# Kernel tuning notes

Measured on AMD Instinct MI355X. Metric: run time of the kernel, lower is better.

## Reference

```python
import jax, jax.numpy as jnp
import numpy as np

D_X = 1024
D_TEXT = 768
FUSION_DIM = D_X + D_TEXT  # 1792
M = 16
K = 2


def setup_inputs() -> dict:
    key = jax.random.key(0)
    k1, k2, k3, k4, k5 = jax.random.split(key, 5)
    B, H, W = 256, 32, 32
    x = jax.random.normal(k1, (B, D_X, H, W), dtype=jnp.float32)
    degraded = jax.random.normal(k2, (B, D_TEXT), dtype=jnp.float32)
    # learned params (random so routing is non-trivial)
    w_fusion = jax.random.normal(k3, (FUSION_DIM, FUSION_DIM), dtype=jnp.float32) * (1.0 / np.sqrt(FUSION_DIM))
    b_fusion = jax.random.normal(k4, (FUSION_DIM,), dtype=jnp.float32) * 0.01
    w_gate = jax.random.normal(k5, (FUSION_DIM, M), dtype=jnp.float32) * 0.02
    return {"x": x, "degraded": degraded, "w_fusion": w_fusion,
            "b_fusion": b_fusion, "w_gate": w_gate}


def reference(x, degraded, w_fusion, b_fusion, w_gate):
    B = x.shape[0]
    # global average pool over H,W -> [B, d_x]
    x_pooled = jnp.mean(x, axis=(2, 3))
    fused = jnp.concatenate([x_pooled, degraded], axis=1)        # [B, d_x+d_text]
    fused = jnp.dot(fused, w_fusion) + b_fusion                  # Linear
    fused = jax.nn.gelu(fused, approximate=False)                # exact GELU (torch default)
    clean_logits = jnp.dot(fused, w_gate)                        # [B, M]
    probs_for_mi = jax.nn.softmax(clean_logits, axis=1)
    # eval path: logits = clean_logits (no noise)
    num_consider = min(K + 1, M)
    top_logits, top_indices = jax.lax.top_k(clean_logits, num_consider)
    top_k_logits = top_logits[:, :K]
    top_k_indices = top_indices[:, :K]
    top_k_gates = jax.nn.softmax(top_k_logits, axis=1)
    rows = jnp.arange(B)[:, None]
    gates = jnp.zeros_like(clean_logits).at[rows, top_k_indices].set(top_k_gates)
    moe_loss = jnp.float32(0.0)
    return gates, moe_loss, probs_for_mi, top_k_indices
```

## Files before the change

kernel.cpp:

```cpp
#include <hip/hip_runtime.h>
#include <math.h>

#define D_X      1024
#define D_TEXT   768
#define FDIM     1792
#define BATCH    256
#define M_EXP    16
#define HW_TOT   1024

#define OUT_GATES 0
#define OUT_LOSS  4096
#define OUT_PROBS 4097
#define OUT_IDX   8193

#define NBLK_DGEMM 224
#define NBLK_POOL  (BATCH * D_X / 4)

__global__ __launch_bounds__(256) void pool_deggemm_kernel(const float* __restrict__ x,
                                                           const float* __restrict__ deg,
                                                           const float* __restrict__ W,
                                                           float* __restrict__ fused,
                                                           float* __restrict__ pact2) {
    __shared__ float As1[32][33];
    __shared__ float Ws1[32][64];

    const int bid = blockIdx.x;
    const int tid = threadIdx.x;

    if (bid >= NBLK_DGEMM) {
        const int gtid = (bid - NBLK_DGEMM) * 256 + tid;
        const int row  = gtid >> 6;
        const int lane = gtid & 63;
        const float4* xr = reinterpret_cast<const float4*>(x + (size_t)row * HW_TOT);
        float s = 0.0f;
#pragma unroll
        for (int k = 0; k < 4; ++k) {
            float4 v = xr[k * 64 + lane];
            s += v.x + v.y + v.z + v.w;
        }
#pragma unroll
        for (int off = 32; off > 0; off >>= 1) s += __shfl_xor(s, off, 64);
        if (lane == 0) fused[row] = s * (1.0f / 1024.0f);
        return;
    }

    const int mb = bid / 28;
    const int nb = bid % 28;
    const int m0 = mb * 32;
    const int n0 = nb * 64;

    const int tx = tid & 15;
    const int ty = tid >> 4;

    const int ar  = tid >> 3;
    const int ak4 = (tid & 7) * 4;
    const int wk  = tid >> 4;
    const int wc4 = (tid & 15) * 4;

    float acc[2][4] = {};

    for (int k0 = 0; k0 < D_TEXT; k0 += 32) {
        __syncthreads();
        {
            const float4 a = *reinterpret_cast<const float4*>(
                deg + (size_t)(m0 + ar) * D_TEXT + k0 + ak4);
            As1[ak4 + 0][ar] = a.x; As1[ak4 + 1][ar] = a.y;
            As1[ak4 + 2][ar] = a.z; As1[ak4 + 3][ar] = a.w;
            *reinterpret_cast<float4*>(&Ws1[wk][wc4]) =
                *reinterpret_cast<const float4*>(W + (size_t)(D_X + k0 + wk) * FDIM + n0 + wc4);
            *reinterpret_cast<float4*>(&Ws1[wk + 16][wc4]) =
                *reinterpret_cast<const float4*>(W + (size_t)(D_X + k0 + wk + 16) * FDIM + n0 + wc4);
        }
        __syncthreads();
#pragma unroll
        for (int kk = 0; kk < 32; ++kk) {
            const float2 a = *reinterpret_cast<const float2*>(&As1[kk][ty * 2]);
            const float4 w = *reinterpret_cast<const float4*>(&Ws1[kk][tx * 4]);
            acc[0][0] = fmaf(a.x, w.x, acc[0][0]);
            acc[0][1] = fmaf(a.x, w.y, acc[0][1]);
            acc[0][2] = fmaf(a.x, w.z, acc[0][2]);
            acc[0][3] = fmaf(a.x, w.w, acc[0][3]);
            acc[1][0] = fmaf(a.y, w.x, acc[1][0]);
            acc[1][1] = fmaf(a.y, w.y, acc[1][1]);
            acc[1][2] = fmaf(a.y, w.z, acc[1][2]);
            acc[1][3] = fmaf(a.y, w.w, acc[1][3]);
        }
    }

#pragma unroll
    for (int i = 0; i < 2; ++i) {
        float4 v;
        v.x = acc[i][0]; v.y = acc[i][1]; v.z = acc[i][2]; v.w = acc[i][3];
        *reinterpret_cast<float4*>(pact2 + (size_t)(m0 + ty * 2 + i) * FDIM + n0 + tx * 4) = v;
    }
}

#define BM 32
#define BN 64
#define BK 64
#define KDIM D_X
#define NITER (KDIM / BK)

#define LOADA(k0)                                                                     \
    pa0 = *reinterpret_cast<const float4*>(A + (size_t)(m0 + ar) * KDIM + (k0) + ak4);       \
    pa1 = *reinterpret_cast<const float4*>(A + (size_t)(m0 + ar + 16) * KDIM + (k0) + ak4);

#define LOADW(k0)                                                                     \
    pw0 = *reinterpret_cast<const float4*>(W + (size_t)((k0) + wr0) * FDIM + n0 + wc4);      \
    pw1 = *reinterpret_cast<const float4*>(W + (size_t)((k0) + wr0 + 16) * FDIM + n0 + wc4); \
    pw2 = *reinterpret_cast<const float4*>(W + (size_t)((k0) + wr0 + 32) * FDIM + n0 + wc4); \
    pw3 = *reinterpret_cast<const float4*>(W + (size_t)((k0) + wr0 + 48) * FDIM + n0 + wc4);

#define STOREA(buf)                                                                   \
    As[buf][ak4 + 0][ar] = pa0.x; As[buf][ak4 + 1][ar] = pa0.y;                       \
    As[buf][ak4 + 2][ar] = pa0.z; As[buf][ak4 + 3][ar] = pa0.w;                       \
    As[buf][ak4 + 0][ar + 16] = pa1.x; As[buf][ak4 + 1][ar + 16] = pa1.y;             \
    As[buf][ak4 + 2][ar + 16] = pa1.z; As[buf][ak4 + 3][ar + 16] = pa1.w;

#define STOREW(buf)                                                                   \
    *reinterpret_cast<float4*>(&Ws[buf][wr0][wc4])      = pw0;                        \
    *reinterpret_cast<float4*>(&Ws[buf][wr0 + 16][wc4]) = pw1;                        \
    *reinterpret_cast<float4*>(&Ws[buf][wr0 + 32][wc4]) = pw2;                        \
    *reinterpret_cast<float4*>(&Ws[buf][wr0 + 48][wc4]) = pw3;

__global__ __launch_bounds__(256) void gemm_gate_kernel(const float* __restrict__ A,
                                                        const float* __restrict__ W,
                                                        const float* __restrict__ pact2,
                                                        const float* __restrict__ bias,
                                                        const float* __restrict__ wg,
                                                        float* __restrict__ part) {
    __shared__ float As[2][BK][BM + 1];
    __shared__ float Ws[2][BK][BN];
    __shared__ float wgs[BN][M_EXP];
    __shared__ float actS[BM][BN + 1];

    const int tid = threadIdx.x;
    const int tx = tid & 15;
    const int ty = tid >> 4;
    const int m0 = blockIdx.x * BM;
    const int n0 = blockIdx.y * BN;

    {
        const int r  = tid >> 2;
        const int c4 = (tid & 3) * 4;
        *reinterpret_cast<float4*>(&wgs[r][c4]) =
            *reinterpret_cast<const float4*>(wg + (size_t)(n0 + r) * M_EXP + c4);
    }

    const int ar  = tid >> 4;
    const int ak4 = (tid & 15) * 4;
    const int wr0 = tid >> 4;
    const int wc4 = (tid & 15) * 4;

    float4 pa0, pa1, pw0, pw1, pw2, pw3;

    LOADA(0); LOADW(0);
    STOREA(0); STOREW(0);
    LOADA(BK); LOADW(BK);

    float acc[2][4];
    {
        const float4 i0 = *reinterpret_cast<const float4*>(
            pact2 + (size_t)(m0 + ty * 2) * FDIM + n0 + tx * 4);
        const float4 i1 = *reinterpret_cast<const float4*>(
            pact2 + (size_t)(m0 + ty * 2 + 1) * FDIM + n0 + tx * 4);
        acc[0][0] = i0.x; acc[0][1] = i0.y; acc[0][2] = i0.z; acc[0][3] = i0.w;
        acc[1][0] = i1.x; acc[1][1] = i1.y; acc[1][2] = i1.z; acc[1][3] = i1.w;
    }
    __syncthreads();

    int cur = 0;
    for (int t = 0; t < NITER; ++t) {
#pragma unroll
        for (int kk = 0; kk < BK; ++kk) {
            const float2 a = *reinterpret_cast<const float2*>(&As[cur][kk][ty * 2]);
            const float4 w = *reinterpret_cast<const float4*>(&Ws[cur][kk][tx * 4]);
            acc[0][0] = fmaf(a.x, w.x, acc[0][0]);
            acc[0][1] = fmaf(a.x, w.y, acc[0][1]);
            acc[0][2] = fmaf(a.x, w.z, acc[0][2]);
            acc[0][3] = fmaf(a.x, w.w, acc[0][3]);
            acc[1][0] = fmaf(a.y, w.x, acc[1][0]);
            acc[1][1] = fmaf(a.y, w.y, acc[1][1]);
            acc[1][2] = fmaf(a.y, w.z, acc[1][2]);
            acc[1][3] = fmaf(a.y, w.w, acc[1][3]);
        }
        if (t < NITER - 1) {
            const int nxt = cur ^ 1;
            STOREA(nxt); STOREW(nxt);
            if (t < NITER - 2) {
                const int k0 = (t + 2) * BK;
                LOADA(k0); LOADW(k0);
            }
            __syncthreads();
            cur = nxt;
        }
    }

#pragma unroll
    for (int i = 0; i < 2; ++i) {
        const int m = ty * 2 + i;
#pragma unroll
        for (int j = 0; j < 4; ++j) {
            const int n = tx * 4 + j;
            const float v = acc[i][j] + bias[n0 + n];
            actS[m][n] = v * 0.5f * (1.0f + erff(v * 0.70710678118654752440f));
        }
    }
    __syncthreads();

    const int pm = tid >> 3;
    const int pe = (tid & 7) * 2;
    float s0 = 0.0f, s1 = 0.0f;
#pragma unroll
    for (int n = 0; n < BN; ++n) {
        const float a = actS[pm][n];
        s0 = fmaf(a, wgs[n][pe], s0);
        s1 = fmaf(a, wgs[n][pe + 1], s1);
    }
    float* pr = part + ((size_t)blockIdx.y * BATCH + m0 + pm) * M_EXP + pe;
    pr[0] = s0;
    pr[1] = s1;
}

#define NNB (FDIM / BN)

__global__ __launch_bounds__(64) void finalize_kernel(const float* __restrict__ part,
                                                      float* __restrict__ out) {
    const int b = blockIdx.x * 64 + threadIdx.x;

    float l[M_EXP];
#pragma unroll
    for (int m = 0; m < M_EXP; ++m) l[m] = 0.0f;

    for (int nb = 0; nb < NNB; ++nb) {
        const float4* pr = reinterpret_cast<const float4*>(part + ((size_t)nb * BATCH + b) * M_EXP);
#pragma unroll
        for (int q = 0; q < 4; ++q) {
            const float4 v = pr[q];
            l[q * 4 + 0] += v.x;
            l[q * 4 + 1] += v.y;
            l[q * 4 + 2] += v.z;
            l[q * 4 + 3] += v.w;
        }
    }

    float mx = l[0];
#pragma unroll
    for (int m = 1; m < M_EXP; ++m) mx = fmaxf(mx, l[m]);
    float e[M_EXP], s = 0.0f;
#pragma unroll
    for (int m = 0; m < M_EXP; ++m) { e[m] = expf(l[m] - mx); s += e[m]; }
    const float inv = 1.0f / s;
#pragma unroll
    for (int m = 0; m < M_EXP; ++m) out[OUT_PROBS + b * M_EXP + m] = e[m] * inv;

    int i0 = 0; float v0 = l[0];
#pragma unroll
    for (int m = 1; m < M_EXP; ++m) if (l[m] > v0) { v0 = l[m]; i0 = m; }
    int i1 = -1; float v1 = -INFINITY;
#pragma unroll
    for (int m = 0; m < M_EXP; ++m) if (m != i0 && l[m] > v1) { v1 = l[m]; i1 = m; }

    const float t = expf(v1 - v0);
    const float g0 = 1.0f / (1.0f + t);
    const float g1 = t * g0;

#pragma unroll
    for (int m = 0; m < M_EXP; ++m) out[OUT_GATES + b * M_EXP + m] = 0.0f;
    out[OUT_GATES + b * M_EXP + i0] = g0;
    out[OUT_GATES + b * M_EXP + i1] = g1;

    out[OUT_IDX + b * 2 + 0] = (float)i0;
    out[OUT_IDX + b * 2 + 1] = (float)i1;

    if (b == 0) out[OUT_LOSS] = 0.0f;
}

extern "C" void kernel_launch(void* const* d_in, const int* in_sizes, int n_in,
                              void* d_out, int out_size, void* d_ws, size_t ws_size,
                              hipStream_t stream) {
    const float* x        = (const float*)d_in[0];
    const float* degraded = (const float*)d_in[1];
    const float* w_fusion = (const float*)d_in[2];
    const float* b_fusion = (const float*)d_in[3];
    const float* w_gate   = (const float*)d_in[4];
    float* out = (float*)d_out;

    float* fused = (float*)d_ws;
    float* pact2 = fused + (size_t)BATCH * D_X;
    float* part  = pact2 + (size_t)BATCH * FDIM;

    pool_deggemm_kernel<<<NBLK_DGEMM + NBLK_POOL, 256, 0, stream>>>(x, degraded, w_fusion,
                                                                   fused, pact2);

    gemm_gate_kernel<<<dim3(BATCH / BM, FDIM / BN), 256, 0, stream>>>(fused, w_fusion, pact2,
                                                                     b_fusion, w_gate, part);

    finalize_kernel<<<BATCH / 64, 64, 0, stream>>>(part, out);
}
```

Baseline: 235.2 us.

## Split-K across waves in gate GEMM and fuse finalize via last-block atomic

The main GEMM kernel now splits each 64-wide K tile across the four waves. Each thread computes a 4x8 register tile, and the partial sums are reduced through shared memory before bias and GELU are applied. The separate finalize kernel is removed: a global atomic counter picks the last block, which then computes the softmax and top-2 gates for all 256 rows. This saves one kernel launch and raises FMA density per LDS load, at the cost of an extra memset, a cross-wave reduction, and a serial tail run by a single block.

```diff
diff --git a/kernel.cpp b/kernel.cpp
--- a/kernel.cpp
+++ b/kernel.cpp
@@ -100,89 +100,87 @@
 #define BK 64
 #define KDIM D_X
 #define NITER (KDIM / BK)
-
-#define LOADA(k0)                                                                     \
+#define ASTR 36
+
+#define AS(buf, k, m) As[(buf) * 2304 + (k) * ASTR + (m)]
+#define WS(buf, k, n) Ws[(buf) * 4096 + (k) * 64 + (n)]
+#define PACC(w, m, n) smem[(w) * 2048 + (m) * 64 + (n)]
+#define ACTS(m, n)    smem[8192 + (m) * 65 + (n)]
+#define WGS(n, e)     smem[10272 + (n) * M_EXP + (e)]
+
+#define LOADA(k0)                                                                            \
     pa0 = *reinterpret_cast<const float4*>(A + (size_t)(m0 + ar) * KDIM + (k0) + ak4);       \
     pa1 = *reinterpret_cast<const float4*>(A + (size_t)(m0 + ar + 16) * KDIM + (k0) + ak4);
 
-#define LOADW(k0)                                                                     \
+#define LOADW(k0)                                                                            \
     pw0 = *reinterpret_cast<const float4*>(W + (size_t)((k0) + wr0) * FDIM + n0 + wc4);      \
     pw1 = *reinterpret_cast<const float4*>(W + (size_t)((k0) + wr0 + 16) * FDIM + n0 + wc4); \
     pw2 = *reinterpret_cast<const float4*>(W + (size_t)((k0) + wr0 + 32) * FDIM + n0 + wc4); \
     pw3 = *reinterpret_cast<const float4*>(W + (size_t)((k0) + wr0 + 48) * FDIM + n0 + wc4);
 
-#define STOREA(buf)                                                                   \
-    As[buf][ak4 + 0][ar] = pa0.x; As[buf][ak4 + 1][ar] = pa0.y;                       \
-    As[buf][ak4 + 2][ar] = pa0.z; As[buf][ak4 + 3][ar] = pa0.w;                       \
-    As[buf][ak4 + 0][ar + 16] = pa1.x; As[buf][ak4 + 1][ar + 16] = pa1.y;             \
-    As[buf][ak4 + 2][ar + 16] = pa1.z; As[buf][ak4 + 3][ar + 16] = pa1.w;
-
-#define STOREW(buf)                                                                   \
-    *reinterpret_cast<float4*>(&Ws[buf][wr0][wc4])      = pw0;                        \
-    *reinterpret_cast<float4*>(&Ws[buf][wr0 + 16][wc4]) = pw1;                        \
-    *reinterpret_cast<float4*>(&Ws[buf][wr0 + 32][wc4]) = pw2;                        \
-    *reinterpret_cast<float4*>(&Ws[buf][wr0 + 48][wc4]) = pw3;
+#define STOREA(buf)                                                                          \
+    AS(buf, ak4 + 0, ar) = pa0.x; AS(buf, ak4 + 1, ar) = pa0.y;                              \
+    AS(buf, ak4 + 2, ar) = pa0.z; AS(buf, ak4 + 3, ar) = pa0.w;                              \
+    AS(buf, ak4 + 0, ar + 16) = pa1.x; AS(buf, ak4 + 1, ar + 16) = pa1.y;                    \
+    AS(buf, ak4 + 2, ar + 16) = pa1.z; AS(buf, ak4 + 3, ar + 16) = pa1.w;
+
+#define STOREW(buf)                                                                          \
+    *reinterpret_cast<float4*>(&WS(buf, wr0, wc4))      = pw0;                               \
+    *reinterpret_cast<float4*>(&WS(buf, wr0 + 16, wc4)) = pw1;                               \
+    *reinterpret_cast<float4*>(&WS(buf, wr0 + 32, wc4)) = pw2;                               \
+    *reinterpret_cast<float4*>(&WS(buf, wr0 + 48, wc4)) = pw3;
 
 __global__ __launch_bounds__(256) void gemm_gate_kernel(const float* __restrict__ A,
                                                         const float* __restrict__ W,
                                                         const float* __restrict__ pact2,
                                                         const float* __restrict__ bias,
                                                         const float* __restrict__ wg,
-                                                        float* __restrict__ part) {
-    __shared__ float As[2][BK][BM + 1];
-    __shared__ float Ws[2][BK][BN];
-    __shared__ float wgs[BN][M_EXP];
-    __shared__ float actS[BM][BN + 1];
+                                                        float* __restrict__ part,
+                                                        int* __restrict__ done,
+                                                        float* __restrict__ out) {
+    __shared__ float smem[12800];
+    __shared__ int isLast;
+    float* As = smem;
+    float* Ws = smem + 4608;
 
     const int tid = threadIdx.x;
-    const int tx = tid & 15;
-    const int ty = tid >> 4;
     const int m0 = blockIdx.x * BM;
     const int n0 = blockIdx.y * BN;
-
-    {
-        const int r  = tid >> 2;
-        const int c4 = (tid & 3) * 4;
-        *reinterpret_cast<float4*>(&wgs[r][c4]) =
-            *reinterpret_cast<const float4*>(wg + (size_t)(n0 + r) * M_EXP + c4);
-    }
 
     const int ar  = tid >> 4;
     const int ak4 = (tid & 15) * 4;
     const int wr0 = tid >> 4;
     const int wc4 = (tid & 15) * 4;
 
+    const int wv   = tid >> 6;
+    const int lane = tid & 63;
+    const int mg   = lane >> 3;
+    const int ng   = lane & 7;
+
     float4 pa0, pa1, pw0, pw1, pw2, pw3;
 
     LOADA(0); LOADW(0);
     STOREA(0); STOREW(0);
     LOADA(BK); LOADW(BK);
-
-    float acc[2][4];
-    {
-        const float4 i0 = *reinterpret_cast<const float4*>(
-            pact2 + (size_t)(m0 + ty * 2) * FDIM + n0 + tx * 4);
-        const float4 i1 = *reinterpret_cast<const float4*>(
-            pact2 + (size_t)(m0 + ty * 2 + 1) * FDIM + n0 + tx * 4);
-        acc[0][0] = i0.x; acc[0][1] = i0.y; acc[0][2] = i0.z; acc[0][3] = i0.w;
-        acc[1][0] = i1.x; acc[1][1] = i1.y; acc[1][2] = i1.z; acc[1][3] = i1.w;
-    }
-    __syncthreads();
-
+    __syncthreads();
+
+    float acc[4][8] = {};
     int cur = 0;
+
     for (int t = 0; t < NITER; ++t) {
 #pragma unroll
-        for (int kk = 0; kk < BK; ++kk) {
-            const float2 a = *reinterpret_cast<const float2*>(&As[cur][kk][ty * 2]);
-            const float4 w = *reinterpret_cast<const float4*>(&Ws[cur][kk][tx * 4]);
-            acc[0][0] = fmaf(a.x, w.x, acc[0][0]);
-            acc[0][1] = fmaf(a.x, w.y, acc[0][1]);
-            acc[0][2] = fmaf(a.x, w.z, acc[0][2]);
-            acc[0][3] = fmaf(a.x, w.w, acc[0][3]);
-            acc[1][0] = fmaf(a.y, w.x, acc[1][0]);
-            acc[1][1] = fmaf(a.y, w.y, acc[1][1]);
-            acc[1][2] = fmaf(a.y, w.z, acc[1][2]);
-            acc[1][3] = fmaf(a.y, w.w, acc[1][3]);
+        for (int s = 0; s < 16; ++s) {
+            const int kk = wv * 16 + s;
+            const float4 a  = *reinterpret_cast<const float4*>(&AS(cur, kk, mg * 4));
+            const float4 w0 = *reinterpret_cast<const float4*>(&WS(cur, kk, ng * 8));
+            const float4 w1 = *reinterpret_cast<const float4*>(&WS(cur, kk, ng * 8 + 4));
+            const float av[4] = {a.x, a.y, a.z, a.w};
+            const float wvv[8] = {w0.x, w0.y, w0.z, w0.w, w1.x, w1.y, w1.z, w1.w};
+#pragma unroll
+            for (int i = 0; i < 4; ++i)
+#pragma unroll
+                for (int j = 0; j < 8; ++j)
+                    acc[i][j] = fmaf(av[i], wvv[j], acc[i][j]);
         }
         if (t < NITER - 1) {
             const int nxt = cur ^ 1;
@@ -196,14 +194,42 @@
         }
     }
 
-#pragma unroll
-    for (int i = 0; i < 2; ++i) {
-        const int m = ty * 2 + i;
-#pragma unroll
-        for (int j = 0; j < 4; ++j) {
-            const int n = tx * 4 + j;
-            const float v = acc[i][j] + bias[n0 + n];
-            actS[m][n] = v * 0.5f * (1.0f + erff(v * 0.70710678118654752440f));
+    __syncthreads();
+
+#pragma unroll
+    for (int i = 0; i < 4; ++i) {
+        float4 v0, v1;
+        v0.x = acc[i][0]; v0.y = acc[i][1]; v0.z = acc[i][2]; v0.w = acc[i][3];
+        v1.x = acc[i][4]; v1.y = acc[i][5]; v1.z = acc[i][6]; v1.w = acc[i][7];
+        *reinterpret_cast<float4*>(&PACC(wv, mg * 4 + i, ng * 8))     = v0;
+        *reinterpret_cast<float4*>(&PACC(wv, mg * 4 + i, ng * 8 + 4)) = v1;
+    }
+    {
+        const int r  = tid >> 2;
+        const int c4 = (tid & 3) * 4;
+        *reinterpret_cast<float4*>(&WGS(r, c4)) =
+            *reinterpret_cast<const float4*>(wg + (size_t)(n0 + r) * M_EXP + c4);
+    }
+    __syncthreads();
+
+    {
+        const int m   = tid >> 3;
+        const int nb8 = (tid & 7) * 8;
+#pragma unroll
+        for (int h = 0; h < 2; ++h) {
+            const int n = nb8 + h * 4;
+            const float4 p  = *reinterpret_cast<const float4*>(
+                pact2 + (size_t)(m0 + m) * FDIM + n0 + n);
+            const float4 bb = *reinterpret_cast<const float4*>(bias + n0 + n);
+            const float pv[4] = {p.x, p.y, p.z, p.w};
+            const float bv[4] = {bb.x, bb.y, bb.z, bb.w};
+#pragma unroll
+            for (int j = 0; j < 4; ++j) {
+                const float v = ((PACC(0, m, n + j) + PACC(1, m, n + j))
+                               + (PACC(2, m, n + j) + PACC(3, m, n + j)))
+                               + pv[j] + bv[j];
+                ACTS(m, n + j) = v * 0.5f * (1.0f + erff(v * 0.70710678118654752440f));
+            }
         }
     }
     __syncthreads();
@@ -213,67 +239,69 @@
     float s0 = 0.0f, s1 = 0.0f;
 #pragma unroll
     for (int n = 0; n < BN; ++n) {
-        const float a = actS[pm][n];
-        s0 = fmaf(a, wgs[n][pe], s0);
-        s1 = fmaf(a, wgs[n][pe + 1], s1);
+        const float a = ACTS(pm, n);
+        s0 = fmaf(a, WGS(n, pe), s0);
+        s1 = fmaf(a, WGS(n, pe + 1), s1);
     }
     float* pr = part + ((size_t)blockIdx.y * BATCH + m0 + pm) * M_EXP + pe;
     pr[0] = s0;
     pr[1] = s1;
-}
-
-#define NNB (FDIM / BN)
-
-__global__ __launch_bounds__(64) void finalize_kernel(const float* __restrict__ part,
-                                                      float* __restrict__ out) {
-    const int b = blockIdx.x * 64 + threadIdx.x;
-
-    float l[M_EXP];
-#pragma unroll
-    for (int m = 0; m < M_EXP; ++m) l[m] = 0.0f;
-
-    for (int nb = 0; nb < NNB; ++nb) {
-        const float4* pr = reinterpret_cast<const float4*>(part + ((size_t)nb * BATCH + b) * M_EXP);
-#pragma unroll
-        for (int q = 0; q < 4; ++q) {
-            const float4 v = pr[q];
-            l[q * 4 + 0] += v.x;
-            l[q * 4 + 1] += v.y;
-            l[q * 4 + 2] += v.z;
-            l[q * 4 + 3] += v.w;
-        }
-    }
-
-    float mx = l[0];
-#pragma unroll
-    for (int m = 1; m < M_EXP; ++m) mx = fmaxf(mx, l[m]);
-    float e[M_EXP], s = 0.0f;
-#pragma unroll
-    for (int m = 0; m < M_EXP; ++m) { e[m] = expf(l[m] - mx); s += e[m]; }
-    const float inv = 1.0f / s;
-#pragma unroll
-    for (int m = 0; m < M_EXP; ++m) out[OUT_PROBS + b * M_EXP + m] = e[m] * inv;
-
-    int i0 = 0; float v0 = l[0];
-#pragma unroll
-    for (int m = 1; m < M_EXP; ++m) if (l[m] > v0) { v0 = l[m]; i0 = m; }
-    int i1 = -1; float v1 = -INFINITY;
-#pragma unroll
-    for (int m = 0; m < M_EXP; ++m) if (m != i0 && l[m] > v1) { v1 = l[m]; i1 = m; }
-
-    const float t = expf(v1 - v0);
-    const float g0 = 1.0f / (1.0f + t);
-    const float g1 = t * g0;
-
-#pragma unroll
-    for (int m = 0; m < M_EXP; ++m) out[OUT_GATES + b * M_EXP + m] = 0.0f;
-    out[OUT_GATES + b * M_EXP + i0] = g0;
-    out[OUT_GATES + b * M_EXP + i1] = g1;
-
-    out[OUT_IDX + b * 2 + 0] = (float)i0;
-    out[OUT_IDX + b * 2 + 1] = (float)i1;
-
-    if (b == 0) out[OUT_LOSS] = 0.0f;
+
+    __threadfence();
+    __syncthreads();
+    if (tid == 0) {
+        const int prev = __hip_atomic_fetch_add(done, 1, __ATOMIC_ACQ_REL,
+                                                __HIP_MEMORY_SCOPE_AGENT);
+        isLast = (prev == 8 * 28 - 1);
+    }
+    __syncthreads();
+    if (!isLast) return;
+
+    {
+        const int b = tid;
+        float l[M_EXP];
+#pragma unroll
+        for (int m = 0; m < M_EXP; ++m) l[m] = 0.0f;
+        for (int nb2 = 0; nb2 < FDIM / BN; ++nb2) {
+            const float4* prr = reinterpret_cast<const float4*>(
+                part + ((size_t)nb2 * BATCH + b) * M_EXP);
+#pragma unroll
+            for (int q = 0; q < 4; ++q) {
+                const float4 v = prr[q];
+                l[q * 4 + 0] += v.x;
+                l[q * 4 + 1] += v.y;
+                l[q * 4 + 2] += v.z;
+                l[q * 4 + 3] += v.w;
+            }
+        }
+        float mx = l[0];
+#pragma unroll
+        for (int m = 1; m < M_EXP; ++m) mx = fmaxf(mx, l[m]);
+        float e[M_EXP], s = 0.0f;
+#pragma unroll
+        for (int m = 0; m < M_EXP; ++m) { e[m] = expf(l[m] - mx); s += e[m]; }
+        const float inv = 1.0f / s;
+#pragma unroll
+        for (int m = 0; m < M_EXP; ++m) out[OUT_PROBS + b * M_EXP + m] = e[m] * inv;
+
+        int i0 = 0; float v0 = l[0];
+#pragma unroll
+        for (int m = 1; m < M_EXP; ++m) if (l[m] > v0) { v0 = l[m]; i0 = m; }
+        int i1 = -1; float v1 = -INFINITY;
+#pragma unroll
+        for (int m = 0; m < M_EXP; ++m) if (m != i0 && l[m] > v1) { v1 = l[m]; i1 = m; }
+
+        const float t = expf(v1 - v0);
+        const float g0 = 1.0f / (1.0f + t);
+        const float g1 = t * g0;
+#pragma unroll
+        for (int m = 0; m < M_EXP; ++m) out[OUT_GATES + b * M_EXP + m] = 0.0f;
+        out[OUT_GATES + b * M_EXP + i0] = g0;
+        out[OUT_GATES + b * M_EXP + i1] = g1;
+        out[OUT_IDX + b * 2 + 0] = (float)i0;
+        out[OUT_IDX + b * 2 + 1] = (float)i1;
+        if (b == 0) out[OUT_LOSS] = 0.0f;
+    }
 }
 
 extern "C" void kernel_launch(void* const* d_in, const int* in_sizes, int n_in,
@@ -289,12 +317,14 @@
     float* fused = (float*)d_ws;
     float* pact2 = fused + (size_t)BATCH * D_X;
     float* part  = pact2 + (size_t)BATCH * FDIM;
+    int*   done  = (int*)(part + (size_t)28 * BATCH * M_EXP);
+
+    hipMemsetAsync(done, 0, sizeof(int), stream);
 
     pool_deggemm_kernel<<<NBLK_DGEMM + NBLK_POOL, 256, 0, stream>>>(x, degraded, w_fusion,
                                                                    fused, pact2);
 
     gemm_gate_kernel<<<dim3(BATCH / BM, FDIM / BN), 256, 0, stream>>>(fused, w_fusion, pact2,
-                                                                     b_fusion, w_gate, part);
-
-    finalize_kernel<<<BATCH / 64, 64, 0, stream>>>(part, out);
+                                                                     b_fusion, w_gate, part,
+                                                                     done, out);
 }
```

Measured after the change: 234.3 us, median of 2. About the same (-0.4%).
